# Optimization experiments

Measured on AMD Instinct MI355X. Metric: run time of the kernel, lower is better.

Reference implementation:

```python
import jax, jax.numpy as jnp
import numpy as np

HEADS = 4
K = 3  # neighborhood kernel size
EPS = 1e-5


def _nbr_idx(dim, k):
    # NATTEN semantics: window start clamped so the full k-window stays in-bounds.
    i = jnp.arange(dim)
    start = jnp.clip(i - k // 2, 0, dim - k)
    return start[:, None] + jnp.arange(k)[None, :]  # [dim, k]


def _gather_windows(t, ix, iy, iz):
    # t: [B, X, Y, Z, n, c] -> [B, X, Y, Z, K^3, n, c]
    t = t[:, ix]                 # [B, X, k, Y, Z, n, c]
    t = t[:, :, :, iy]           # [B, X, k, Y, k, Z, n, c]
    t = t[:, :, :, :, :, iz]     # [B, X, k, Y, k, Z, k, n, c]
    t = t.transpose(0, 1, 3, 5, 2, 4, 6, 7, 8)  # [B,X,Y,Z,k,k,k,n,c]
    B, X, Y, Z = t.shape[0], t.shape[1], t.shape[2], t.shape[3]
    return t.reshape(B, X, Y, Z, K * K * K, HEADS, -1)


def setup_inputs() -> dict:
    key = jax.random.key(0)
    k1, k2, k3 = jax.random.split(key, 3)
    C = 128
    x = jax.random.normal(k1, (1, C, 32, 32, 32), dtype=jnp.float32)
    ln_gamma = jnp.ones((C,), jnp.float32)
    ln_beta = jnp.zeros((C,), jnp.float32)
    qkv_w = jax.random.normal(k2, (3 * C, C), dtype=jnp.float32) * 0.02
    qkv_b = jnp.zeros((3 * C,), jnp.float32)
    proj_w = jax.random.normal(k3, (C, C), dtype=jnp.float32) * 0.02
    proj_b = jnp.zeros((C,), jnp.float32)
    return {"x": x, "ln_gamma": ln_gamma, "ln_beta": ln_beta,
            "qkv_w": qkv_w, "qkv_b": qkv_b, "proj_w": proj_w, "proj_b": proj_b}


def reference(x, ln_gamma, ln_beta, qkv_w, qkv_b, proj_w, proj_b):
    B, C, X, Y, Z = x.shape
    hd = C // HEADS
    scale = hd ** -0.5

    # permute to channels-last + LayerNorm over C
    h = x.transpose(0, 2, 3, 4, 1)  # [B,X,Y,Z,C]
    mu = jnp.mean(h, axis=-1, keepdims=True)
    var = jnp.mean(jnp.square(h - mu), axis=-1, keepdims=True)
    h = (h - mu) * jax.lax.rsqrt(var + EPS) * ln_gamma + ln_beta

    # QKV projection
    qkv = h @ qkv_w.T + qkv_b                     # [B,X,Y,Z,3C]
    q, k, v = jnp.split(qkv, 3, axis=-1)
    q = q.reshape(B, X, Y, Z, HEADS, hd)
    k = k.reshape(B, X, Y, Z, HEADS, hd)
    v = v.reshape(B, X, Y, Z, HEADS, hd)

    ix, iy, iz = _nbr_idx(X, K), _nbr_idx(Y, K), _nbr_idx(Z, K)
    k_win = _gather_windows(k, ix, iy, iz)  # [B,X,Y,Z,27,n,hd]
    v_win = _gather_windows(v, ix, iy, iz)

    attn = jnp.einsum('bxyznc,bxyzknc->bxyznk', q * scale, k_win)
    attn = jax.nn.softmax(attn, axis=-1)
    out = jnp.einsum('bxyznk,bxyzknc->bxyznc', attn, v_win)
    out = out.reshape(B, X, Y, Z, C)

    out = out @ proj_w.T + proj_b                 # output projection
    return out.transpose(0, 4, 1, 2, 3) + x      # residual, channels-first
```

## Files before the change

kernel.cpp:

```cpp
#include <hip/hip_runtime.h>

#define N_VOX 32768
#define CCH 128
#define EPSV 1e-5f

typedef __attribute__((ext_vector_type(8))) short bfrag;
typedef __attribute__((ext_vector_type(4))) float ffrag;
typedef __attribute__((ext_vector_type(2))) unsigned int u32x2;

__device__ __forceinline__ float bf2f(unsigned short u) {
    union { unsigned int i; float f; } c; c.i = ((unsigned int)u) << 16; return c.f;
}
__device__ __forceinline__ unsigned short f2bf(float f) {
    union { float f; unsigned int i; } c; c.f = f;
    unsigned int i = c.i;
    return (unsigned short)((i + 0x7FFFu + ((i >> 16) & 1u)) >> 16);
}
__device__ __forceinline__ unsigned int cvtpk(float lo, float hi) {
    unsigned int r;
    asm("v_cvt_pk_bf16_f32 %0, %1, %2" : "=v"(r) : "v"(lo), "v"(hi));
    return r;
}

__global__ __launch_bounds__(256) void ln_qkv(const float* __restrict__ x,
                                              const float* __restrict__ gamma,
                                              const float* __restrict__ beta,
                                              const float* __restrict__ w,
                                              const float* __restrict__ bias,
                                              unsigned short* __restrict__ qkv) {
    __shared__ __align__(16) unsigned short a_s[64 * 136];
    __shared__ __align__(16) unsigned short b_s[64 * 136];
    __shared__ float ps[256], pq[256];
    __shared__ float muS[64], rsS[64];
    __shared__ float g[128], bta[128];
    int t = threadIdx.x;
    int og = blockIdx.x;
    int v0 = blockIdx.y * 64;
    if (t < 128) { g[t] = gamma[t]; bta[t] = beta[t]; }
    int cq = t >> 6, v = t & 63;
    float xr[32];
    float s = 0.f, sq = 0.f;
    #pragma unroll
    for (int i = 0; i < 32; i++) {
        float val = x[(size_t)(cq * 32 + i) * N_VOX + v0 + v];
        xr[i] = val; s += val; sq += val * val;
    }
    ps[t] = s; pq[t] = sq;
    __syncthreads();
    if (t < 64) {
        float S = ps[t] + ps[t + 64] + ps[t + 128] + ps[t + 192];
        float Q = pq[t] + pq[t + 64] + pq[t + 128] + pq[t + 192];
        float mu = S * (1.0f / 128.0f);
        float var = Q * (1.0f / 128.0f) - mu * mu;
        muS[t] = mu; rsS[t] = rsqrtf(var + EPSV);
    }
    __syncthreads();
    {
        float mu = muS[v], rs = rsS[v];
        #pragma unroll
        for (int i8 = 0; i8 < 4; i8++) {
            float val[8];
            #pragma unroll
            for (int k = 0; k < 8; k++) {
                int c = cq * 32 + i8 * 8 + k;
                val[k] = (xr[i8 * 8 + k] - mu) * rs * g[c] + bta[c];
            }
            uint4 q;
            q.x = cvtpk(val[0], val[1]);
            q.y = cvtpk(val[2], val[3]);
            q.z = cvtpk(val[4], val[5]);
            q.w = cvtpk(val[6], val[7]);
            *(uint4*)&a_s[v * 136 + cq * 32 + i8 * 8] = q;
        }
    }
    __syncthreads();
    int lane = t & 63, wvi = t >> 6, m = lane & 15, quad = lane >> 4;
    bfrag areg[4];
    #pragma unroll
    for (int kk = 0; kk < 4; kk++)
        areg[kk] = *(bfrag*)&a_s[(wvi * 16 + m) * 136 + kk * 32 + quad * 8];
    for (int t0 = 0; t0 < 3; t0++) {
        int o0 = og * 192 + t0 * 64;
        {
            int r4 = t >> 4, c8 = t & 15;
            #pragma unroll
            for (int pass = 0; pass < 4; pass++) {
                int r = pass * 16 + r4;
                float4 w0 = *(const float4*)&w[(size_t)(o0 + r) * 128 + c8 * 8];
                float4 w1 = *(const float4*)&w[(size_t)(o0 + r) * 128 + c8 * 8 + 4];
                uint4 q;
                q.x = cvtpk(w0.x, w0.y);
                q.y = cvtpk(w0.z, w0.w);
                q.z = cvtpk(w1.x, w1.y);
                q.w = cvtpk(w1.z, w1.w);
                *(uint4*)&b_s[r * 136 + c8 * 8] = q;
            }
        }
        __syncthreads();
        ffrag acc[4] = {ffrag{0,0,0,0}, ffrag{0,0,0,0}, ffrag{0,0,0,0}, ffrag{0,0,0,0}};
        #pragma unroll
        for (int kk = 0; kk < 4; kk++) {
            #pragma unroll
            for (int nt = 0; nt < 4; nt++) {
                bfrag bb = *(bfrag*)&b_s[(nt * 16 + m) * 136 + kk * 32 + quad * 8];
                acc[nt] = __builtin_amdgcn_mfma_f32_16x16x32_bf16(areg[kk], bb, acc[nt], 0, 0, 0);
            }
        }
        bool isq = (o0 < 128);
        #pragma unroll
        for (int nt = 0; nt < 4; nt++) {
            int o = o0 + nt * 16 + m;
            float bs = bias[o];
            int sec = o >> 7;
            int oc = o & 127;
            unsigned short* dst = qkv + (size_t)sec * ((size_t)N_VOX * 128);
            #pragma unroll
            for (int r = 0; r < 4; r++) {
                int vg = v0 + wvi * 16 + quad * 4 + r;
                float val = acc[nt][r] + bs;
                if (isq) val *= 0.17677669529663687f;
                dst[(size_t)vg * 128 + oc] = f2bf(val);
            }
        }
        __syncthreads();
    }
}

#define VT_STRIDE 188
__global__ __launch_bounds__(256) void attn_kernel(const unsigned short* __restrict__ qb,
                                                   const unsigned short* __restrict__ kb,
                                                   const unsigned short* __restrict__ vb,
                                                   unsigned short* __restrict__ ob) {
    __shared__ unsigned int vjtab[176];
    __shared__ __align__(16) unsigned short vt[4][32 * VT_STRIDE];

    int t = threadIdx.x;
    int hw = blockIdx.x;
    int bidx = (hw & 7) * 256 + (hw >> 3);
    int zh = bidx & 1, yy = (bidx >> 1) & 31, xx = bidx >> 6;
    int z0 = zh << 4;
    int sx = min(max(xx - 1, 0), 29);
    int sy = min(max(yy - 1, 0), 29);
    int zr0 = min(max(z0 - 1, 0), 14);
    int vox0 = (xx << 10) + (yy << 5) + z0;

    if (t < 176) {
        int r = t < 162 ? t : 161;
        int rxy = r / 18;
        int rzv = r - rxy * 18;
        int ax = rxy / 3;
        int by = rxy - ax * 3;
        vjtab[t] = (unsigned)(((sx + ax) << 10) + ((sy + by) << 5) + (zr0 + rzv));
    }
    __syncthreads();

    int wave = t >> 6, lane = t & 63;
    int hq = lane >> 4;
    int m = lane & 15;
    int ch0 = wave * 32;

    unsigned short* vts = &vt[wave][0];
    {
        const int cp = m;
        #pragma unroll
        for (int u = 0; u < 11; u++) {
            int rb = u * 16 + hq * 4;
            unsigned int j0 = vjtab[rb + 0];
            unsigned int j1 = vjtab[rb + 1];
            unsigned int j2 = vjtab[rb + 2];
            unsigned int j3 = vjtab[rb + 3];
            unsigned int d0 = *(const unsigned int*)&vb[(size_t)j0 * 128 + ch0 + cp * 2];
            unsigned int d1 = *(const unsigned int*)&vb[(size_t)j1 * 128 + ch0 + cp * 2];
            unsigned int d2 = *(const unsigned int*)&vb[(size_t)j2 * 128 + ch0 + cp * 2];
            unsigned int d3 = *(const unsigned int*)&vb[(size_t)j3 * 128 + ch0 + cp * 2];
            if (u == 10) {
                if (rb + 0 >= 162) d0 = 0u;
                if (rb + 1 >= 162) d1 = 0u;
                if (rb + 2 >= 162) d2 = 0u;
                if (rb + 3 >= 162) d3 = 0u;
            }
            unsigned int lo01 = __builtin_amdgcn_perm(d1, d0, 0x05040100u);
            unsigned int lo23 = __builtin_amdgcn_perm(d3, d2, 0x05040100u);
            unsigned int hi01 = __builtin_amdgcn_perm(d1, d0, 0x07060302u);
            unsigned int hi23 = __builtin_amdgcn_perm(d3, d2, 0x07060302u);
            u32x2 wlo; wlo.x = lo01; wlo.y = lo23;
            u32x2 whi; whi.x = hi01; whi.y = hi23;
            *(u32x2*)&vts[(2 * cp) * VT_STRIDE + rb] = wlo;
            *(u32x2*)&vts[(2 * cp + 1) * VT_STRIDE + rb] = whi;
        }
    }

    bfrag qf = *(const bfrag*)&qb[(size_t)(vox0 + m) * 128 + ch0 + hq * 8];
    ffrag s[11];
    #pragma unroll
    for (int f = 0; f < 11; f++) {
        unsigned int vj = vjtab[f * 16 + m];
        bfrag kf = *(const bfrag*)&kb[(size_t)vj * 128 + ch0 + hq * 8];
        s[f] = __builtin_amdgcn_mfma_f32_16x16x32_bf16(kf, qf, ffrag{0,0,0,0}, 0, 0, 0);
    }

    int zv = z0 + m;
    int szv = min(max(zv - 1, 0), 29);
    unsigned int wz = (unsigned int)(szv - zr0);
    unsigned int rz = 4u * (unsigned int)hq;
    float mx = -1e30f;
    #pragma unroll
    for (int f = 0; f < 11; f++) {
        #pragma unroll
        for (int i = 0; i < 4; i++) {
            unsigned int ri = rz + (unsigned int)i;
            ri = min(ri, ri - 18u);
            bool valid = (ri - wz) <= 2u;
            if (f == 10) valid = valid && ((4 * hq + i) < 2);
            float sv = valid ? s[f][i] : -1e30f;
            s[f][i] = sv;
            mx = fmaxf(mx, sv);
        }
        rz = min(rz + 16u, rz - 2u);
    }
    mx = fmaxf(mx, __shfl_xor(mx, 16));
    mx = fmaxf(mx, __shfl_xor(mx, 32));
    float sum = 0.f;
    #pragma unroll
    for (int f = 0; f < 11; f++) {
        #pragma unroll
        for (int i = 0; i < 4; i++) {
            float p = __expf(s[f][i] - mx);
            s[f][i] = p;
            sum += p;
        }
    }
    sum += __shfl_xor(sum, 16);
    sum += __shfl_xor(sum, 32);
    float inv = 1.0f / sum;

    ffrag acc0 = ffrag{0,0,0,0};
    ffrag acc1 = ffrag{0,0,0,0};
    const unsigned short* ab = &vt[wave][m * VT_STRIDE + hq * 4];
    #pragma unroll
    for (int f = 0; f < 11; f++) {
        u32x2 pb; pb.x = cvtpk(s[f][0], s[f][1]); pb.y = cvtpk(s[f][2], s[f][3]);
        u32x2 av0 = *(const u32x2*)&ab[f * 16];
        u32x2 av1 = *(const u32x2*)&ab[16 * VT_STRIDE + f * 16];
        asm("v_mfma_f32_16x16x16_bf16 %0, %1, %2, %0" : "+v"(acc0) : "v"(av0), "v"(pb));
        asm("v_mfma_f32_16x16x16_bf16 %0, %1, %2, %0" : "+v"(acc1) : "v"(av1), "v"(pb));
    }

    size_t obase = (size_t)(vox0 + m) * 128 + ch0 + hq * 4;
    {
        u32x2 ov;
        ov.x = cvtpk(acc0[0] * inv, acc0[1] * inv);
        ov.y = cvtpk(acc0[2] * inv, acc0[3] * inv);
        *(u32x2*)&ob[obase] = ov;
    }
    {
        u32x2 ov;
        ov.x = cvtpk(acc1[0] * inv, acc1[1] * inv);
        ov.y = cvtpk(acc1[2] * inv, acc1[3] * inv);
        *(u32x2*)&ob[obase + 16] = ov;
    }
}

__global__ __launch_bounds__(256) void proj_gemm(const unsigned short* __restrict__ a,
                                                 const float* __restrict__ w,
                                                 const float* __restrict__ bias,
                                                 const float* __restrict__ xres,
                                                 float* __restrict__ out) {
    __shared__ __align__(16) unsigned short a_s[64 * 136];
    __shared__ __align__(16) unsigned short b_s[64 * 136];
    int t = threadIdx.x;
    int m0 = blockIdx.x * 64, o0 = blockIdx.y * 64;
    {
        int r4 = t >> 4, c8 = t & 15;
        #pragma unroll
        for (int pass = 0; pass < 4; pass++) {
            int r = pass * 16 + r4;
            *(uint4*)&a_s[r * 136 + c8 * 8] =
                *(const uint4*)&a[(size_t)(m0 + r) * 128 + c8 * 8];
            float4 w0 = *(const float4*)&w[(size_t)(o0 + r) * 128 + c8 * 8];
            float4 w1 = *(const float4*)&w[(size_t)(o0 + r) * 128 + c8 * 8 + 4];
            uint4 q;
            q.x = cvtpk(w0.x, w0.y);
            q.y = cvtpk(w0.z, w0.w);
            q.z = cvtpk(w1.x, w1.y);
            q.w = cvtpk(w1.z, w1.w);
            *(uint4*)&b_s[r * 136 + c8 * 8] = q;
        }
    }
    __syncthreads();
    int wvi = t >> 6, lane = t & 63, m = lane & 15, quad = lane >> 4;
    ffrag acc[4] = {ffrag{0,0,0,0}, ffrag{0,0,0,0}, ffrag{0,0,0,0}, ffrag{0,0,0,0}};
    #pragma unroll
    for (int kk = 0; kk < 4; kk++) {
        bfrag av = *(bfrag*)&a_s[(wvi * 16 + m) * 136 + kk * 32 + quad * 8];
        #pragma unroll
        for (int nt = 0; nt < 4; nt++) {
            bfrag bb = *(bfrag*)&b_s[(nt * 16 + m) * 136 + kk * 32 + quad * 8];
            acc[nt] = __builtin_amdgcn_mfma_f32_16x16x32_bf16(av, bb, acc[nt], 0, 0, 0);
        }
    }
    #pragma unroll
    for (int nt = 0; nt < 4; nt++) {
        int o = o0 + nt * 16 + m;
        float bs = bias[o];
        int vg = m0 + wvi * 16 + quad * 4;
        float4 r = *(const float4*)&xres[(size_t)o * N_VOX + vg];
        float4 ov;
        ov.x = acc[nt][0] + bs + r.x;
        ov.y = acc[nt][1] + bs + r.y;
        ov.z = acc[nt][2] + bs + r.z;
        ov.w = acc[nt][3] + bs + r.w;
        *(float4*)&out[(size_t)o * N_VOX + vg] = ov;
    }
}

extern "C" void kernel_launch(void* const* d_in, const int* in_sizes, int n_in,
                              void* d_out, int out_size, void* d_ws, size_t ws_size,
                              hipStream_t stream) {
    const float* x      = (const float*)d_in[0];
    const float* gamma  = (const float*)d_in[1];
    const float* beta   = (const float*)d_in[2];
    const float* qkv_w  = (const float*)d_in[3];
    const float* qkv_b  = (const float*)d_in[4];
    const float* proj_w = (const float*)d_in[5];
    const float* proj_b = (const float*)d_in[6];
    float* out = (float*)d_out;

    unsigned short* qkv  = (unsigned short*)d_ws;
    unsigned short* attn = (unsigned short*)((char*)d_ws + (24u << 20));

    hipLaunchKernelGGL(ln_qkv, dim3(2, 512), dim3(256), 0, stream,
                       x, gamma, beta, qkv_w, qkv_b, qkv);
    const unsigned short* qb = qkv;
    const unsigned short* kb = qkv + (size_t)N_VOX * 128;
    const unsigned short* vb = qkv + (size_t)2 * N_VOX * 128;
    hipLaunchKernelGGL(attn_kernel, dim3(2048), dim3(256), 0, stream, qb, kb, vb, attn);
    hipLaunchKernelGGL(proj_gemm, dim3(512, 2), dim3(256), 0, stream, attn, proj_w, proj_b, x, out);
}
```

Before: 118.2 us.

## Tile attention queries as 2x2x4 voxel blocks to shrink the key/value halo

Each block of 16 query voxels now covers a 2x2x4 cube instead of a 1x1x16 z-line. This cuts the neighborhood union from 162 to 96 key/value voxels, so the kernel does 6 MFMA fragments and gathers instead of 11. Validity masks are precomputed into a shared-memory bitmask table, replacing the inline z-range arithmetic. The cost is a per-block mask setup and a more scattered voxel layout for the q loads and output stores.

Result: faster. 112.6 us (-4.8%).

```diff
diff --git a/kernel.cpp b/kernel.cpp
--- a/kernel.cpp
+++ b/kernel.cpp
@@ -126,31 +126,51 @@
     }
 }
 
-#define VT_STRIDE 188
+#define VT2 100
 __global__ __launch_bounds__(256) void attn_kernel(const unsigned short* __restrict__ qb,
                                                    const unsigned short* __restrict__ kb,
                                                    const unsigned short* __restrict__ vb,
                                                    unsigned short* __restrict__ ob) {
-    __shared__ unsigned int vjtab[176];
-    __shared__ __align__(16) unsigned short vt[4][32 * VT_STRIDE];
+    __shared__ unsigned int vjtab[96];
+    __shared__ __align__(16) unsigned int vmsk[96];
+    __shared__ __align__(16) unsigned short vt[4][32 * VT2];
 
     int t = threadIdx.x;
     int hw = blockIdx.x;
     int bidx = (hw & 7) * 256 + (hw >> 3);
-    int zh = bidx & 1, yy = (bidx >> 1) & 31, xx = bidx >> 6;
-    int z0 = zh << 4;
-    int sx = min(max(xx - 1, 0), 29);
-    int sy = min(max(yy - 1, 0), 29);
-    int zr0 = min(max(z0 - 1, 0), 14);
-    int vox0 = (xx << 10) + (yy << 5) + z0;
-
-    if (t < 176) {
-        int r = t < 162 ? t : 161;
-        int rxy = r / 18;
-        int rzv = r - rxy * 18;
-        int ax = rxy / 3;
-        int by = rxy - ax * 3;
-        vjtab[t] = (unsigned)(((sx + ax) << 10) + ((sy + by) << 5) + (zr0 + rzv));
+    int czi = bidx & 7, cyi = (bidx >> 3) & 15, cxi = bidx >> 7;
+    int cx0 = cxi << 1, cy0 = cyi << 1, cz0 = czi << 2;
+    int rx0 = min(max(cx0 - 1, 0), 28);
+    int ry0 = min(max(cy0 - 1, 0), 28);
+    int rz0 = min(max(cz0 - 1, 0), 26);
+
+    if (t < 96) {
+        int r = t;
+        int ax = r / 24;
+        int rem = r - ax * 24;
+        int by = rem / 6;
+        int cz = rem - by * 6;
+        vjtab[t] = (unsigned)(((rx0 + ax) << 10) + ((ry0 + by) << 5) + (rz0 + cz));
+        int wx0 = min(max(cx0 - 1, 0), 29) - rx0;
+        int wx1 = min(cx0, 29) - rx0;
+        int wy0 = min(max(cy0 - 1, 0), 29) - ry0;
+        int wy1 = min(cy0, 29) - ry0;
+        unsigned zn = 0;
+        #pragma unroll
+        for (int vz = 0; vz < 4; vz++) {
+            int wz = min(max(cz0 + vz - 1, 0), 29) - rz0;
+            if ((unsigned)(cz - wz) <= 2u) zn |= 1u << vz;
+        }
+        bool x0 = (unsigned)(ax - wx0) <= 2u;
+        bool x1 = (unsigned)(ax - wx1) <= 2u;
+        bool y0 = (unsigned)(by - wy0) <= 2u;
+        bool y1 = (unsigned)(by - wy1) <= 2u;
+        unsigned msk = 0;
+        if (x0 && y0) msk |= zn;
+        if (x0 && y1) msk |= zn << 4;
+        if (x1 && y0) msk |= zn << 8;
+        if (x1 && y1) msk |= zn << 12;
+        vmsk[t] = msk;
     }
     __syncthreads();
 
@@ -163,7 +183,7 @@
     {
         const int cp = m;
         #pragma unroll
-        for (int u = 0; u < 11; u++) {
+        for (int u = 0; u < 6; u++) {
             int rb = u * 16 + hq * 4;
             unsigned int j0 = vjtab[rb + 0];
             unsigned int j1 = vjtab[rb + 1];
@@ -173,56 +193,47 @@
             unsigned int d1 = *(const unsigned int*)&vb[(size_t)j1 * 128 + ch0 + cp * 2];
             unsigned int d2 = *(const unsigned int*)&vb[(size_t)j2 * 128 + ch0 + cp * 2];
             unsigned int d3 = *(const unsigned int*)&vb[(size_t)j3 * 128 + ch0 + cp * 2];
-            if (u == 10) {
-                if (rb + 0 >= 162) d0 = 0u;
-                if (rb + 1 >= 162) d1 = 0u;
-                if (rb + 2 >= 162) d2 = 0u;
-                if (rb + 3 >= 162) d3 = 0u;
-            }
             unsigned int lo01 = __builtin_amdgcn_perm(d1, d0, 0x05040100u);
             unsigned int lo23 = __builtin_amdgcn_perm(d3, d2, 0x05040100u);
             unsigned int hi01 = __builtin_amdgcn_perm(d1, d0, 0x07060302u);
             unsigned int hi23 = __builtin_amdgcn_perm(d3, d2, 0x07060302u);
             u32x2 wlo; wlo.x = lo01; wlo.y = lo23;
             u32x2 whi; whi.x = hi01; whi.y = hi23;
-            *(u32x2*)&vts[(2 * cp) * VT_STRIDE + rb] = wlo;
-            *(u32x2*)&vts[(2 * cp + 1) * VT_STRIDE + rb] = whi;
-        }
-    }
-
-    bfrag qf = *(const bfrag*)&qb[(size_t)(vox0 + m) * 128 + ch0 + hq * 8];
-    ffrag s[11];
-    #pragma unroll
-    for (int f = 0; f < 11; f++) {
+            *(u32x2*)&vts[(2 * cp) * VT2 + rb] = wlo;
+            *(u32x2*)&vts[(2 * cp + 1) * VT2 + rb] = whi;
+        }
+    }
+
+    int gx = cx0 + (m >> 3), gy = cy0 + ((m >> 2) & 1), gz = cz0 + (m & 3);
+    int vox = (gx << 10) + (gy << 5) + gz;
+
+    bfrag qf = *(const bfrag*)&qb[(size_t)vox * 128 + ch0 + hq * 8];
+    ffrag s[6];
+    #pragma unroll
+    for (int f = 0; f < 6; f++) {
         unsigned int vj = vjtab[f * 16 + m];
         bfrag kf = *(const bfrag*)&kb[(size_t)vj * 128 + ch0 + hq * 8];
         s[f] = __builtin_amdgcn_mfma_f32_16x16x32_bf16(kf, qf, ffrag{0,0,0,0}, 0, 0, 0);
     }
 
-    int zv = z0 + m;
-    int szv = min(max(zv - 1, 0), 29);
-    unsigned int wz = (unsigned int)(szv - zr0);
-    unsigned int rz = 4u * (unsigned int)hq;
     float mx = -1e30f;
     #pragma unroll
-    for (int f = 0; f < 11; f++) {
+    for (int f = 0; f < 6; f++) {
+        uint4 mk = *(const uint4*)&vmsk[f * 16 + hq * 4];
+        unsigned mm[4] = {mk.x, mk.y, mk.z, mk.w};
         #pragma unroll
         for (int i = 0; i < 4; i++) {
-            unsigned int ri = rz + (unsigned int)i;
-            ri = min(ri, ri - 18u);
-            bool valid = (ri - wz) <= 2u;
-            if (f == 10) valid = valid && ((4 * hq + i) < 2);
+            bool valid = (mm[i] >> m) & 1u;
             float sv = valid ? s[f][i] : -1e30f;
             s[f][i] = sv;
             mx = fmaxf(mx, sv);
         }
-        rz = min(rz + 16u, rz - 2u);
     }
     mx = fmaxf(mx, __shfl_xor(mx, 16));
     mx = fmaxf(mx, __shfl_xor(mx, 32));
     float sum = 0.f;
     #pragma unroll
-    for (int f = 0; f < 11; f++) {
+    for (int f = 0; f < 6; f++) {
         #pragma unroll
         for (int i = 0; i < 4; i++) {
             float p = __expf(s[f][i] - mx);
@@ -236,17 +247,17 @@
 
     ffrag acc0 = ffrag{0,0,0,0};
     ffrag acc1 = ffrag{0,0,0,0};
-    const unsigned short* ab = &vt[wave][m * VT_STRIDE + hq * 4];
-    #pragma unroll
-    for (int f = 0; f < 11; f++) {
+    const unsigned short* ab = &vt[wave][m * VT2 + hq * 4];
+    #pragma unroll
+    for (int f = 0; f < 6; f++) {
         u32x2 pb; pb.x = cvtpk(s[f][0], s[f][1]); pb.y = cvtpk(s[f][2], s[f][3]);
         u32x2 av0 = *(const u32x2*)&ab[f * 16];
-        u32x2 av1 = *(const u32x2*)&ab[16 * VT_STRIDE + f * 16];
+        u32x2 av1 = *(const u32x2*)&ab[16 * VT2 + f * 16];
         asm("v_mfma_f32_16x16x16_bf16 %0, %1, %2, %0" : "+v"(acc0) : "v"(av0), "v"(pb));
         asm("v_mfma_f32_16x16x16_bf16 %0, %1, %2, %0" : "+v"(acc1) : "v"(av1), "v"(pb));
     }
 
-    size_t obase = (size_t)(vox0 + m) * 128 + ch0 + hq * 4;
+    size_t obase = (size_t)vox * 128 + ch0 + hq * 4;
     {
         u32x2 ov;
         ov.x = cvtpk(acc0[0] * inv, acc0[1] * inv);
```
